# Kernel tuning notes

Hardware: AMD Instinct MI355X
Metric: run time of the kernel (lower is better)

## Reference

```python
import jax, jax.numpy as jnp
import numpy as np


def setup_inputs() -> dict:
    key = jax.random.key(0)
    k1, k2, k3 = jax.random.split(key, 3)
    B, C, H, W = 32, 192, 64, 64
    L = 64  # number of unique quantization levels in the sos codebook
    x = jax.random.normal(k1, (B, C, H, W), dtype=jnp.float32) * 4.0
    means = jax.random.normal(k2, (B, C, H, W), dtype=jnp.float32)
    # sorted 1-D codebook of unique quantizer levels (sos.unique_values)
    codebook = jnp.sort(jax.random.normal(k3, (L,), dtype=jnp.float32) * 4.0)
    return {"x": x, "means": means, "codebook": codebook}


def _nearest_level(r, codebook):
    """Vectorized version of transform_map: for each element of r, the index of
    the nearest codebook value (argmin |codebook - r|), using searchsorted on
    the sorted codebook instead of a dense [N, L] distance matrix."""
    L = codebook.shape[0]
    pos = jnp.clip(jnp.searchsorted(codebook, r), 1, L - 1)  # right neighbor
    left = codebook[pos - 1]
    right = codebook[pos]
    return jnp.where(r - left <= right - r, pos - 1, pos)  # int32 symbols


def reference(x, means, codebook):
    # quantize(mode='symbols'): subtract means, map each value to the index of
    # the nearest codebook level (the map_sos_cdf dict lookup / argmin loop).
    r = x - means
    symbols = _nearest_level(r, codebook)          # [B,C,H,W] int32
    # dequantize: map symbols back to float levels (map_cdf_sos) and add means.
    y_hat = jnp.take(codebook, symbols) + means    # [B,C,H,W] float32
    return symbols, y_hat
```

## Files before the change

### kernel.cpp

```cpp
#include <hip/hip_runtime.h>


typedef float v4f __attribute__((ext_vector_type(4)));

__device__ __forceinline__ void nearest(const float* __restrict__ s_cb,
                                        float r, float m,
                                        float& sym, float& y)
{
    int p = 0;
#pragma unroll
    for (int s = 32; s > 0; s >>= 1) {
        p += (s_cb[p + s - 1] < r) ? s : 0;
    }
    p = min(max(p, 1), 63);
    const float left  = s_cb[p - 1];
    const float right = s_cb[p];
    const int idx = ((r - left) <= (right - r)) ? (p - 1) : p;
    sym = (float)idx;
    y   = s_cb[idx] + m;
}

__global__ __launch_bounds__(256) void quant_dequant_kernel(
    const v4f* __restrict__ x4,
    const v4f* __restrict__ m4,
    const float* __restrict__ codebook,
    v4f* __restrict__ sym_out,
    v4f* __restrict__ yhat_out,
    int n8)
{
    __shared__ float s_cb[64];
    if (threadIdx.x < 64) s_cb[threadIdx.x] = codebook[threadIdx.x];
    __syncthreads();

    const int i = blockIdx.x * blockDim.x + threadIdx.x;
    if (i >= n8) return;
    const int j = i + n8;

    const v4f xa = x4[i];
    const v4f ma = m4[i];
    const v4f xb = x4[j];
    const v4f mb = m4[j];

    v4f sa, ya, sb, yb;
#pragma unroll
    for (int k = 0; k < 4; ++k) {
        float s0, y0, s1, y1;
        nearest(s_cb, xa[k] - ma[k], ma[k], s0, y0);
        nearest(s_cb, xb[k] - mb[k], mb[k], s1, y1);
        sa[k] = s0; ya[k] = y0;
        sb[k] = s1; yb[k] = y1;
    }

    __builtin_nontemporal_store(sa, &sym_out[i]);
    __builtin_nontemporal_store(ya, &yhat_out[i]);
    __builtin_nontemporal_store(sb, &sym_out[j]);
    __builtin_nontemporal_store(yb, &yhat_out[j]);
}

extern "C" void kernel_launch(void* const* d_in, const int* in_sizes, int n_in,
                              void* d_out, int out_size, void* d_ws, size_t ws_size,
                              hipStream_t stream)
{
    const float* x     = (const float*)d_in[0];
    const float* means = (const float*)d_in[1];
    const float* cb    = (const float*)d_in[2];

    const int n  = in_sizes[0];
    const int n8 = n / 8;

    float* out = (float*)d_out;

    const int block = 256;
    const int grid  = (n8 + block - 1) / block;

    quant_dequant_kernel<<<grid, block, 0, stream>>>(
        (const v4f*)x, (const v4f*)means, cb,
        (v4f*)out, (v4f*)(out + n), n8);
}
```

Baseline: 343.4 us.

## Replace LDS binary search with register tree and wavefront shuffles

The first four levels of the codebook binary search now use register-resident pivot values selected with conditional moves. The last levels and the neighbor lookups use cross-lane shuffles of a per-lane codebook copy instead of shared memory. This removes the shared-memory staging, the block barrier, and most dependent LDS reads, including the dequantize lookup, which now reuses the left/right values. It adds register pressure and an occupancy hint, and the shuffles assume all lanes in the wavefront are active.

```diff
diff --git a/kernel.cpp b/kernel.cpp
--- a/kernel.cpp
+++ b/kernel.cpp
@@ -3,24 +3,50 @@
 
 typedef float v4f __attribute__((ext_vector_type(4)));
 
-__device__ __forceinline__ void nearest(const float* __restrict__ s_cb,
+struct Tree {
+    float c31;
+    float c15, c47;
+    float c07, c23, c39, c55;
+    float c03, c11, c19, c27, c35, c43, c51, c59;
+};
+
+__device__ __forceinline__ void nearest(const Tree& t, float cbreg,
                                         float r, float m,
                                         float& sym, float& y)
 {
-    int p = 0;
-#pragma unroll
-    for (int s = 32; s > 0; s >>= 1) {
-        p += (s_cb[p + s - 1] < r) ? s : 0;
-    }
+    int p = (t.c31 < r) ? 32 : 0;
+
+    float v = (p & 32) ? t.c47 : t.c15;
+    p += (v < r) ? 16 : 0;
+
+    float u0 = (p & 16) ? t.c23 : t.c07;
+    float u1 = (p & 16) ? t.c55 : t.c39;
+    v = (p & 32) ? u1 : u0;
+    p += (v < r) ? 8 : 0;
+
+    float w0 = (p & 8) ? t.c11 : t.c03;
+    float w1 = (p & 8) ? t.c27 : t.c19;
+    float w2 = (p & 8) ? t.c43 : t.c35;
+    float w3 = (p & 8) ? t.c59 : t.c51;
+    float w4 = (p & 16) ? w1 : w0;
+    float w5 = (p & 16) ? w3 : w2;
+    v = (p & 32) ? w5 : w4;
+    p += (v < r) ? 4 : 0;
+
+    v = __shfl(cbreg, p + 1);
+    p += (v < r) ? 2 : 0;
+    v = __shfl(cbreg, p);
+    p += (v < r) ? 1 : 0;
+
     p = min(max(p, 1), 63);
-    const float left  = s_cb[p - 1];
-    const float right = s_cb[p];
-    const int idx = ((r - left) <= (right - r)) ? (p - 1) : p;
-    sym = (float)idx;
-    y   = s_cb[idx] + m;
+    const float left  = __shfl(cbreg, p - 1);
+    const float right = __shfl(cbreg, p);
+    const bool tie = (r - left) <= (right - r);
+    sym = (float)(tie ? p - 1 : p);
+    y   = (tie ? left : right) + m;
 }
 
-__global__ __launch_bounds__(256) void quant_dequant_kernel(
+__global__ __launch_bounds__(256, 4) void quant_dequant_kernel(
     const v4f* __restrict__ x4,
     const v4f* __restrict__ m4,
     const float* __restrict__ codebook,
@@ -28,9 +54,17 @@
     v4f* __restrict__ yhat_out,
     int n8)
 {
-    __shared__ float s_cb[64];
-    if (threadIdx.x < 64) s_cb[threadIdx.x] = codebook[threadIdx.x];
-    __syncthreads();
+    const float cbreg = codebook[threadIdx.x & 63];
+
+    Tree t;
+    t.c31 = codebook[31];
+    t.c15 = codebook[15]; t.c47 = codebook[47];
+    t.c07 = codebook[7];  t.c23 = codebook[23];
+    t.c39 = codebook[39]; t.c55 = codebook[55];
+    t.c03 = codebook[3];  t.c11 = codebook[11];
+    t.c19 = codebook[19]; t.c27 = codebook[27];
+    t.c35 = codebook[35]; t.c43 = codebook[43];
+    t.c51 = codebook[51]; t.c59 = codebook[59];
 
     const int i = blockIdx.x * blockDim.x + threadIdx.x;
     if (i >= n8) return;
@@ -45,8 +79,8 @@
 #pragma unroll
     for (int k = 0; k < 4; ++k) {
         float s0, y0, s1, y1;
-        nearest(s_cb, xa[k] - ma[k], ma[k], s0, y0);
-        nearest(s_cb, xb[k] - mb[k], mb[k], s1, y1);
+        nearest(t, cbreg, xa[k] - ma[k], ma[k], s0, y0);
+        nearest(t, cbreg, xb[k] - mb[k], mb[k], s1, y1);
         sa[k] = s0; ya[k] = y0;
         sb[k] = s1; yb[k] = y1;
     }
```

After: 345.4 us. No clear change (+0.6%).
